# Optimization experiments

Measured on AMD Instinct MI355X. Metric: run time of the kernel, lower is better.

## Reference

```python
import jax, jax.numpy as jnp
import numpy as np

BINS = 10

def setup_inputs() -> dict:
    key = jax.random.key(0)
    k1, k2 = jax.random.split(key)
    N, C = 262144, 512
    x = jax.random.normal(k1, (N, C), dtype=jnp.float32)
    target = jax.random.randint(k2, (N,), 0, C, dtype=jnp.int64)
    return {"x": x, "target": target}

def reference(x, target):
    # log-softmax + NLL (reduction='none', no class weights)
    log_p = jax.nn.log_softmax(x, axis=-1)                      # [N, C]
    log_pt = jnp.take_along_axis(log_p, target[:, None].astype(jnp.int32), axis=1)[:, 0]  # [N]
    ce = -log_pt                                                # NLL per-sample
    # gradient-norm proxy g = |pt - 1|, detached
    g = jax.lax.stop_gradient(jnp.abs(jnp.exp(log_pt) - 1.0))   # [N]
    bin_idx = jnp.floor(g * (BINS - 0.0001)).astype(jnp.int32)  # [N] in [0, BINS)
    # histogram (first call: _last_bin_count is None -> raw counts, no EMA)
    bin_count = jnp.zeros((BINS,), dtype=x.dtype).at[bin_idx].add(1.0)
    nonempty = jnp.sum(bin_count > 0).astype(x.dtype)
    gd = jnp.maximum(bin_count * nonempty, 0.0001)
    beta = 1.0 / gd                                             # [BINS]
    loss = jax.lax.stop_gradient(beta[bin_idx]) * ce            # [N]
    return loss.mean()                                          # reduction='mean'
```

## Files before the change

### kernel.cpp

```cpp
#include <hip/hip_runtime.h>
#include <hip/hip_bf16.h>

#define BINS 10
#define C 512
#define NBLK 2048


__device__ __forceinline__ void process_row(const float* __restrict__ rowp,
                                            const float4 (&v)[8],
                                            int sub, int tgt,
                                            float* s_cnt, float* s_sum) {
    float xt = rowp[tgt];
    float s = 0.0f;
    #pragma unroll
    for (int j = 0; j < 8; ++j)
        s += __expf(v[j].x) + __expf(v[j].y) + __expf(v[j].z) + __expf(v[j].w);
    #pragma unroll
    for (int off = 8; off >= 1; off >>= 1)
        s += __shfl_xor(s, off);
    float lse = __logf(s);
    float ce  = lse - xt;
    float pt  = __expf(xt - lse);
    float g   = fabsf(pt - 1.0f);
    int   bin = (int)(g * (BINS - 0.0001f));
    bin = bin < 0 ? 0 : (bin > BINS - 1 ? BINS - 1 : bin);
    if (sub == 0) {
        atomicAdd(&s_cnt[bin], 1.0f);
        atomicAdd(&s_sum[bin], ce);
    }
}

__global__ __launch_bounds__(256, 2) void ghmc_pass1(const float* __restrict__ x,
                                                     const int* __restrict__ target,
                                                     float* __restrict__ slots,
                                                     int N) {
    __shared__ float s_cnt[BINS];
    __shared__ float s_sum[BINS];
    const int tid = threadIdx.x;
    if (tid < BINS) { s_cnt[tid] = 0.0f; s_sum[tid] = 0.0f; }
    __syncthreads();

    const int sub    = tid & 15;
    const int grp    = tid >> 4;
    const int row0   = blockIdx.x * 16 + grp;
    const int stride = gridDim.x * 16;

    for (int row = row0; row < N; row += 2 * stride) {
        const int rowB = row + stride;
        const bool hasB = rowB < N;

        const float* rowpA = x + (size_t)row * C;
        const float4* rpA  = (const float4*)rowpA;
        int tgtA = target[row];
        float4 a[8];
        #pragma unroll
        for (int j = 0; j < 8; ++j) a[j] = rpA[sub + 16 * j];

        const float* rowpB = x + (size_t)rowB * C;
        const float4* rpB  = (const float4*)rowpB;
        int tgtB = 0;
        float4 b[8];
        if (hasB) {
            tgtB = target[rowB];
            #pragma unroll
            for (int j = 0; j < 8; ++j) b[j] = rpB[sub + 16 * j];
        }

        process_row(rowpA, a, sub, tgtA, s_cnt, s_sum);
        if (hasB)
            process_row(rowpB, b, sub, tgtB, s_cnt, s_sum);
    }

    __syncthreads();
    if (tid < BINS) {
        slots[blockIdx.x * 2 * BINS + tid]        = s_cnt[tid];
        slots[blockIdx.x * 2 * BINS + BINS + tid] = s_sum[tid];
    }
}

__global__ __launch_bounds__(256) void ghmc_pass2(const float* __restrict__ slots,
                                                  float* __restrict__ out,
                                                  int nblk, float invN) {
    __shared__ float red[256][2 * BINS];
    const int tid = threadIdx.x;

    float c[2 * BINS];
    #pragma unroll
    for (int k = 0; k < 2 * BINS; ++k) c[k] = 0.0f;

    for (int b = tid; b < nblk; b += 256) {
        const float* sp = slots + (size_t)b * 2 * BINS;
        #pragma unroll
        for (int k = 0; k < 2 * BINS; ++k) c[k] += sp[k];
    }
    #pragma unroll
    for (int k = 0; k < 2 * BINS; ++k) red[tid][k] = c[k];
    __syncthreads();

    for (int off = 128; off >= 1; off >>= 1) {
        if (tid < off) {
            #pragma unroll
            for (int k = 0; k < 2 * BINS; ++k)
                red[tid][k] += red[tid + off][k];
        }
        __syncthreads();
    }

    if (tid == 0) {
        int ne = 0;
        #pragma unroll
        for (int b = 0; b < BINS; ++b)
            if (red[0][b] > 0.0f) ne++;
        float nef = (float)ne;
        float acc = 0.0f;
        #pragma unroll
        for (int b = 0; b < BINS; ++b) {
            float gd = fmaxf(red[0][b] * nef, 0.0001f);
            acc += red[0][BINS + b] / gd;
        }
        out[0] = acc * invN;
    }
}

extern "C" void kernel_launch(void* const* d_in, const int* in_sizes, int n_in,
                              void* d_out, int out_size, void* d_ws, size_t ws_size,
                              hipStream_t stream) {
    const float* x      = (const float*)d_in[0];
    const int*   target = (const int*)d_in[1];
    float*       out    = (float*)d_out;
    float*       slots  = (float*)d_ws;

    const int N = in_sizes[1];

    int nblk = NBLK;
    size_t need = (size_t)nblk * 2 * BINS * sizeof(float);
    if (ws_size < need) {
        nblk = (int)(ws_size / (2 * BINS * sizeof(float)));
        if (nblk < 1) nblk = 1;
    }

    ghmc_pass1<<<nblk, 256, 0, stream>>>(x, target, slots, N);
    ghmc_pass2<<<1, 256, 0, stream>>>(slots, out, nblk, 1.0f / (float)N);
}
```

Before: 99.92 us.

## Software-pipeline row loads so next A row prefetches during B compute

Restructures the pass-1 loop into a rolling double buffer. Row A is loaded before the loop, and the next A row is issued right after processing the current A, so its global loads overlap with row B's exp/reduce work. The target logit load is also hoisted next to the row loads. This raises live register pressure and could reduce occupancy at the existing launch bounds.

```diff
diff --git a/kernel.cpp b/kernel.cpp
--- a/kernel.cpp
+++ b/kernel.cpp
@@ -6,11 +6,9 @@
 #define NBLK 2048
 
 
-__device__ __forceinline__ void process_row(const float* __restrict__ rowp,
-                                            const float4 (&v)[8],
-                                            int sub, int tgt,
+__device__ __forceinline__ void process_row(const float4 (&v)[8], float xt,
+                                            int sub,
                                             float* s_cnt, float* s_sum) {
-    float xt = rowp[tgt];
     float s = 0.0f;
     #pragma unroll
     for (int j = 0; j < 8; ++j)
@@ -45,30 +43,43 @@
     const int row0   = blockIdx.x * 16 + grp;
     const int stride = gridDim.x * 16;
 
+    float4 a[8];
+    float  xtA = 0.0f;
+    if (row0 < N) {
+        const float4* rp = (const float4*)(x + (size_t)row0 * C);
+        int t = target[row0];
+        #pragma unroll
+        for (int j = 0; j < 8; ++j) a[j] = rp[sub + 16 * j];
+        xtA = x[(size_t)row0 * C + t];
+    }
+
     for (int row = row0; row < N; row += 2 * stride) {
         const int rowB = row + stride;
         const bool hasB = rowB < N;
 
-        const float* rowpA = x + (size_t)row * C;
-        const float4* rpA  = (const float4*)rowpA;
-        int tgtA = target[row];
-        float4 a[8];
-        #pragma unroll
-        for (int j = 0; j < 8; ++j) a[j] = rpA[sub + 16 * j];
-
-        const float* rowpB = x + (size_t)rowB * C;
-        const float4* rpB  = (const float4*)rowpB;
-        int tgtB = 0;
         float4 b[8];
+        float  xtB = 0.0f;
         if (hasB) {
-            tgtB = target[rowB];
+            const float4* rp = (const float4*)(x + (size_t)rowB * C);
+            int t = target[rowB];
             #pragma unroll
-            for (int j = 0; j < 8; ++j) b[j] = rpB[sub + 16 * j];
+            for (int j = 0; j < 8; ++j) b[j] = rp[sub + 16 * j];
+            xtB = x[(size_t)rowB * C + t];
         }
 
-        process_row(rowpA, a, sub, tgtA, s_cnt, s_sum);
+        process_row(a, xtA, sub, s_cnt, s_sum);
+
+        const int rowN2 = row + 2 * stride;
+        if (rowN2 < N) {
+            const float4* rp = (const float4*)(x + (size_t)rowN2 * C);
+            int t = target[rowN2];
+            #pragma unroll
+            for (int j = 0; j < 8; ++j) a[j] = rp[sub + 16 * j];
+            xtA = x[(size_t)rowN2 * C + t];
+        }
+
         if (hasB)
-            process_row(rowpB, b, sub, tgtB, s_cnt, s_sum);
+            process_row(b, xtB, sub, s_cnt, s_sum);
     }
 
     __syncthreads();
```

Result: no change. 98.79 us, median of 2 (-1.1%).

## Switch to wave-per-row batches with software-pipelined double-buffered loads

Applied to the files above, without the earlier changes.

Each 64-lane wavefront now handles batches of 4 consecutive rows, with each lane holding two float4 per row, in place of 16-lane groups per row. Loads for the next batch are issued before the current batch is processed, ping-ponging between two register buffers so memory latency overlaps the exp and reduction work. This adds a 6-step shuffle reduction per row and keeps more registers live, which could lower occupancy.

```diff
diff --git a/kernel.cpp b/kernel.cpp
--- a/kernel.cpp
+++ b/kernel.cpp
@@ -5,30 +5,6 @@
 #define C 512
 #define NBLK 2048
 
-
-__device__ __forceinline__ void process_row(const float* __restrict__ rowp,
-                                            const float4 (&v)[8],
-                                            int sub, int tgt,
-                                            float* s_cnt, float* s_sum) {
-    float xt = rowp[tgt];
-    float s = 0.0f;
-    #pragma unroll
-    for (int j = 0; j < 8; ++j)
-        s += __expf(v[j].x) + __expf(v[j].y) + __expf(v[j].z) + __expf(v[j].w);
-    #pragma unroll
-    for (int off = 8; off >= 1; off >>= 1)
-        s += __shfl_xor(s, off);
-    float lse = __logf(s);
-    float ce  = lse - xt;
-    float pt  = __expf(xt - lse);
-    float g   = fabsf(pt - 1.0f);
-    int   bin = (int)(g * (BINS - 0.0001f));
-    bin = bin < 0 ? 0 : (bin > BINS - 1 ? BINS - 1 : bin);
-    if (sub == 0) {
-        atomicAdd(&s_cnt[bin], 1.0f);
-        atomicAdd(&s_sum[bin], ce);
-    }
-}
 
 __global__ __launch_bounds__(256, 2) void ghmc_pass1(const float* __restrict__ x,
                                                      const int* __restrict__ target,
@@ -40,35 +16,65 @@
     if (tid < BINS) { s_cnt[tid] = 0.0f; s_sum[tid] = 0.0f; }
     __syncthreads();
 
-    const int sub    = tid & 15;
-    const int grp    = tid >> 4;
-    const int row0   = blockIdx.x * 16 + grp;
-    const int stride = gridDim.x * 16;
+    const int lane = tid & 63;
+    const int wav  = tid >> 6;
+    const int gw   = blockIdx.x * 4 + wav;
+    const int nw   = gridDim.x * 4;
+    const int step = 4 * nw;
 
-    for (int row = row0; row < N; row += 2 * stride) {
-        const int rowB = row + stride;
-        const bool hasB = rowB < N;
+    auto load_batch = [&](int rbase, float4 (&v)[8], float (&xt)[4]) {
+        #pragma unroll
+        for (int k = 0; k < 4; ++k) {
+            const int row = rbase + k;
+            if (row < N) {
+                const float4* rp = (const float4*)(x + (size_t)row * C);
+                v[2 * k]     = rp[lane];
+                v[2 * k + 1] = rp[lane + 64];
+                xt[k] = x[(size_t)row * C + target[row]];
+            }
+        }
+    };
 
-        const float* rowpA = x + (size_t)row * C;
-        const float4* rpA  = (const float4*)rowpA;
-        int tgtA = target[row];
-        float4 a[8];
+    auto process_batch = [&](int rbase, const float4 (&v)[8], const float (&xt)[4]) {
         #pragma unroll
-        for (int j = 0; j < 8; ++j) a[j] = rpA[sub + 16 * j];
+        for (int k = 0; k < 4; ++k) {
+            const int row = rbase + k;
+            if (row >= N) break;
+            const float4 p = v[2 * k], q = v[2 * k + 1];
+            float s = __expf(p.x) + __expf(p.y) + __expf(p.z) + __expf(p.w)
+                    + __expf(q.x) + __expf(q.y) + __expf(q.z) + __expf(q.w);
+            #pragma unroll
+            for (int off = 32; off >= 1; off >>= 1)
+                s += __shfl_xor(s, off);
+            float lse = __logf(s);
+            float ce  = lse - xt[k];
+            float pt  = __expf(xt[k] - lse);
+            float g   = fabsf(pt - 1.0f);
+            int   bin = (int)(g * (BINS - 0.0001f));
+            bin = bin < 0 ? 0 : (bin > BINS - 1 ? BINS - 1 : bin);
+            if (lane == 0) {
+                atomicAdd(&s_cnt[bin], 1.0f);
+                atomicAdd(&s_sum[bin], ce);
+            }
+        }
+    };
 
-        const float* rowpB = x + (size_t)rowB * C;
-        const float4* rpB  = (const float4*)rowpB;
-        int tgtB = 0;
-        float4 b[8];
-        if (hasB) {
-            tgtB = target[rowB];
-            #pragma unroll
-            for (int j = 0; j < 8; ++j) b[j] = rpB[sub + 16 * j];
-        }
+    float4 a[8]; float xtA[4];
+    float4 b[8]; float xtB[4];
 
-        process_row(rowpA, a, sub, tgtA, s_cnt, s_sum);
-        if (hasB)
-            process_row(rowpB, b, sub, tgtB, s_cnt, s_sum);
+    int rb = 4 * gw;
+    if (rb < N) load_batch(rb, a, xtA);
+
+    for (; rb < N; rb += 2 * step) {
+        const int rbB = rb + step;
+        if (rbB < N) load_batch(rbB, b, xtB);
+
+        process_batch(rb, a, xtA);
+
+        const int rbN = rb + 2 * step;
+        if (rbN < N) load_batch(rbN, a, xtA);
+
+        if (rbB < N) process_batch(rbB, b, xtB);
     }
 
     __syncthreads();
```

After: 100.3 us. No clear change (+0.3%).
